# Kernel optimization log

Hardware: AMD Instinct MI355X
Metric: run time of the kernel (lower is better)

The kernel has to match this reference:

```python
import jax, jax.numpy as jnp
import numpy as np
import math

N_HEADS = 16
D_MODEL = 1024
DK = D_MODEL // N_HEADS
B, S = 2, 2048


def setup_inputs() -> dict:
    key = jax.random.key(0)
    ks = jax.random.split(key, 11)
    scale_in = 1.0 / math.sqrt(D_MODEL)
    scale_o = 1.0 / math.sqrt(N_HEADS * DK)
    return {
        "query": jax.random.normal(ks[0], (B, S, D_MODEL), jnp.float32),
        "key": jax.random.normal(ks[1], (B, S, D_MODEL), jnp.float32),
        "value": jax.random.normal(ks[2], (B, S, D_MODEL), jnp.float32),
        # stacked per-head projection weights [H, d_model, dk], biases [H, dk]
        "Wq": jax.random.normal(ks[3], (N_HEADS, D_MODEL, DK), jnp.float32) * scale_in,
        "bq": jax.random.normal(ks[4], (N_HEADS, DK), jnp.float32) * scale_in,
        "Wk": jax.random.normal(ks[5], (N_HEADS, D_MODEL, DK), jnp.float32) * scale_in,
        "bk": jax.random.normal(ks[6], (N_HEADS, DK), jnp.float32) * scale_in,
        "Wv": jax.random.normal(ks[7], (N_HEADS, D_MODEL, DK), jnp.float32) * scale_in,
        "bv": jax.random.normal(ks[8], (N_HEADS, DK), jnp.float32) * scale_in,
        "Wo": jax.random.normal(ks[9], (N_HEADS * DK, D_MODEL), jnp.float32) * scale_o,
        "bo": jax.random.normal(ks[10], (D_MODEL,), jnp.float32) * scale_o,
    }


def reference(query, key, value, Wq, bq, Wk, bk, Wv, bv, Wo, bo):
    # Per-head linear projections, vectorized over heads: [B,H,S,dk]
    q = jnp.einsum("bsd,hdk->bhsk", query, Wq) + bq[None, :, None, :]
    k = jnp.einsum("bsd,hdk->bhsk", key, Wk) + bk[None, :, None, :]
    v = jnp.einsum("bsd,hdk->bhsk", value, Wv) + bv[None, :, None, :]
    # Scaled dot-product scores [B,H,S,S]
    scores = jnp.einsum("bhsk,bhtk->bhst", q, k) / jnp.sqrt(jnp.asarray(DK, q.dtype))
    # FAITHFUL to source: nn.Softmax(dim=0) -> softmax over the BATCH axis
    attn = jax.nn.softmax(scores, axis=0)
    out = jnp.einsum("bhst,bhtk->bhsk", attn, v)  # [B,H,S,dk]
    # concat heads along feature dim (torch.cat dim=2)
    concat = out.transpose(0, 2, 1, 3).reshape(query.shape[0], query.shape[1], N_HEADS * DK)
    return concat @ Wo + bo
```

## Files before the change

### kernel.cpp

```cpp
#include <hip/hip_runtime.h>
#include <hip/hip_bf16.h>

#define B_ 2
#define S_ 2048
#define D_ 1024
#define H_ 16
#define DK_ 64
#define BS_ (B_ * S_)

typedef unsigned int u32;
typedef unsigned short u16;
typedef __attribute__((ext_vector_type(8))) short bf16x8;
typedef __attribute__((ext_vector_type(4))) float f32x4;

typedef const __attribute__((address_space(1))) void glb_cv;
typedef __attribute__((address_space(3))) void lds_v;

__device__ __forceinline__ void async_cp16(const void* g, void* l) {
    __builtin_amdgcn_global_load_lds((glb_cv*)g, (lds_v*)l, 16, 0, 0);
}

__device__ __forceinline__ float bf2f(u16 v) {
    union { u32 u; float f; } c; c.u = ((u32)v) << 16; return c.f;
}
__device__ __forceinline__ u16 f2bf(float f) {
    union { float f; u32 u; } c; c.f = f;
    u32 u = c.u;
    return (u16)((u + 0x7fffu + ((u >> 16) & 1u)) >> 16);
}
__device__ __forceinline__ u32 pack2(float a, float b) {
    return (u32)f2bf(a) | ((u32)f2bf(b) << 16);
}
__device__ __forceinline__ u32 packtr(float lo, float hi) {
    union { float f; u32 u; } a, b; a.f = lo; b.f = hi;
    return __builtin_amdgcn_perm(b.u, a.u, 0x07060302u);
}
__device__ __forceinline__ int sw64(int r, int c8) { return (((c8) + (r)) & 7) * 8; }

struct PrepArgs {
    const float* W[4]; u16* WT[4];
    const float* X[3]; u16* XB[3];
};
__global__ __launch_bounds__(256) void prep(PrepArgs a)
{
    const int id = blockIdx.x;
    const int tid = threadIdx.x;
    if (id >= 1024) {
        const int cid = id - 1024;
        const int z = cid >> 11;
        const size_t base = (size_t)(cid & 2047) * 2048 + tid * 8;
        const float* X = a.X[z];
        float4 x0 = *(const float4*)(X + base);
        float4 x1 = *(const float4*)(X + base + 4);
        uint4 o;
        o.x = pack2(x0.x, x0.y); o.y = pack2(x0.z, x0.w);
        o.z = pack2(x1.x, x1.y); o.w = pack2(x1.z, x1.w);
        *(uint4*)(a.XB[z] + base) = o;
        return;
    }
    __shared__ __attribute__((aligned(16))) u16 T[64][72];
    const int z = id >> 8;
    const int rem = id & 255;
    const float* W = a.W[z];
    u16* WT = a.WT[z];
    const int headMode = (z < 3) ? 1 : 0;
    const int k0 = (rem >> 4) * 64;
    const int n0 = (rem & 15) * 64;
    const int kr = tid >> 4;
    const int n4 = (tid & 15) * 4;
    #pragma unroll
    for (int pass = 0; pass < 4; ++pass) {
        int kk = k0 + pass * 16 + kr;
        const float* p = headMode
            ? (W + (size_t)((n0 + n4) >> 6) * (1024 * 64) + kk * 64 + ((n0 + n4) & 63))
            : (W + (size_t)kk * 1024 + n0 + n4);
        float4 v = *(const float4*)p;
        int krel = pass * 16 + kr;
        T[n4 + 0][krel] = f2bf(v.x);
        T[n4 + 1][krel] = f2bf(v.y);
        T[n4 + 2][krel] = f2bf(v.z);
        T[n4 + 3][krel] = f2bf(v.w);
    }
    __syncthreads();
    const int nr = tid >> 2;
    const int kq = (tid & 3) * 16;
    uint4 o0 = *(const uint4*)&T[nr][kq];
    uint4 o1 = *(const uint4*)&T[nr][kq + 8];
    u16* q = WT + (size_t)(n0 + nr) * 1024 + k0 + kq;
    *(uint4*)q = o0;
    *(uint4*)(q + 8) = o1;
}

__global__ __launch_bounds__(256) void vprep(
    const u16* __restrict__ Vb, u16* __restrict__ VT)
{
    __shared__ __attribute__((aligned(16))) u16 T[64][72];
    const int tid = threadIdx.x;
    const int t0 = blockIdx.x * 64;
    const int bh = blockIdx.y;
    const int b = bh >> 4, h = bh & 15;
    const int tr = tid >> 4;
    const int d4 = (tid & 15) * 4;
    #pragma unroll
    for (int pass = 0; pass < 4; ++pass) {
        int tt = t0 + pass * 16 + tr;
        const u16* p = Vb + (size_t)(b * S_ + tt) * 1024 + h * 64 + d4;
        u32 a = *(const u32*)p;
        u32 c = *(const u32*)(p + 2);
        int trel = pass * 16 + tr;
        T[d4 + 0][trel] = (u16)a;
        T[d4 + 1][trel] = (u16)(a >> 16);
        T[d4 + 2][trel] = (u16)c;
        T[d4 + 3][trel] = (u16)(c >> 16);
    }
    __syncthreads();
    const int dr = tid >> 2;
    const int tq = (tid & 3) * 16;
    uint4 o0 = *(const uint4*)&T[dr][tq];
    uint4 o1 = *(const uint4*)&T[dr][tq + 8];
    u16* q = VT + ((size_t)bh * 64 + dr) * 2048 + t0 + tq;
    *(uint4*)q = o0;
    *(uint4*)(q + 8) = o1;
}

struct ProjArgs {
    const u16* X[3];
    const u16* W[3];
    const float* bias[3];
    u16* Y[3];
};
__global__ __launch_bounds__(256) void proj3(ProjArgs pa)
{
    __shared__ __attribute__((aligned(16))) u16 As[128][32];
    __shared__ __attribute__((aligned(16))) u16 Bs[128][32];
    const int z = blockIdx.z;
    const u16* X = pa.X[z];
    const u16* WT = pa.W[z];
    const float* bias = pa.bias[z];
    u16* Y = pa.Y[z];
    const int neg = (z == 1);

    const int tid = threadIdx.x;
    const int lane = tid & 63;
    const int wave = tid >> 6;
    const int quad = lane >> 4;
    const int l16 = lane & 15;
    const int m0 = blockIdx.x * 128;
    const int n0 = blockIdx.y * 128;
    const int wm = (wave & 1) * 64, wn = (wave >> 1) * 64;

    f32x4 acc[4][4] = {};

    for (int k0 = 0; k0 < 1024; k0 += 32) {
        __syncthreads();
        #pragma unroll
        for (int call = 0; call < 2; ++call) {
            const int c = tid + call * 256;
            const int row = c >> 2, cc = (c & 3) * 8;
            char* la = (char*)&As[0][0] + (size_t)(c & ~63) * 16;
            async_cp16(X + (size_t)(m0 + row) * 1024 + k0 + cc, la);
            char* lb = (char*)&Bs[0][0] + (size_t)(c & ~63) * 16;
            async_cp16(WT + (size_t)(n0 + row) * 1024 + k0 + cc, lb);
        }
        __syncthreads();

        bf16x8 af[4], bfr[4];
        #pragma unroll
        for (int mt = 0; mt < 4; ++mt)
            af[mt] = *(const bf16x8*)&As[wm + mt * 16 + l16][quad * 8];
        #pragma unroll
        for (int nt = 0; nt < 4; ++nt)
            bfr[nt] = *(const bf16x8*)&Bs[wn + nt * 16 + l16][quad * 8];
        #pragma unroll
        for (int mt = 0; mt < 4; ++mt)
            #pragma unroll
            for (int nt = 0; nt < 4; ++nt)
                acc[mt][nt] = __builtin_amdgcn_mfma_f32_16x16x32_bf16(
                    af[mt], bfr[nt], acc[mt][nt], 0, 0, 0);
    }

    #pragma unroll
    for (int nt = 0; nt < 4; ++nt) {
        const int col = n0 + wn + nt * 16 + l16;
        const float bv = bias[col];
        #pragma unroll
        for (int mt = 0; mt < 4; ++mt) {
            #pragma unroll
            for (int r = 0; r < 4; ++r) {
                const int row = m0 + wm + mt * 16 + quad * 4 + r;
                float v = acc[mt][nt][r] + bv;
                if (neg && row >= 2048) v = -v;
                Y[(size_t)row * 1024 + col] = f2bf(v);
            }
        }
    }
}

__global__ __launch_bounds__(256) void gemm_out(
    const u16* __restrict__ P0, const u16* __restrict__ P1,
    const float* __restrict__ csP,
    const u16* __restrict__ WT, const float* __restrict__ bias,
    float* __restrict__ Y)
{
    __shared__ __attribute__((aligned(16))) u16 Aa[128][32];
    __shared__ __attribute__((aligned(16))) u16 Ab[128][32];
    __shared__ __attribute__((aligned(16))) u16 As[128][32];
    __shared__ __attribute__((aligned(16))) u16 Bs[64][32];
    __shared__ __attribute__((aligned(16))) float csL[1024];

    const int tid = threadIdx.x;
    const int lane = tid & 63;
    const int wave = tid >> 6;
    const int quad = lane >> 4;
    const int l16 = lane & 15;
    const int m0 = blockIdx.x * 128;
    const int n0 = blockIdx.y * 64;
    const int wm = (wave & 1) * 64, wn = (wave >> 1) * 32;
    const bool hiB = (m0 >= 2048);

    {
        const int t4 = tid * 4;
        float4 c0 = *(const float4*)(csP + t4);
        float4 c1 = *(const float4*)(csP + 1024 + t4);
        csL[t4 + 0] = c0.x + c1.x;
        csL[t4 + 1] = c0.y + c1.y;
        csL[t4 + 2] = c0.z + c1.z;
        csL[t4 + 3] = c0.w + c1.w;
    }

    f32x4 acc[4][2] = {};

    for (int k0 = 0; k0 < 1024; k0 += 32) {
        __syncthreads();
        #pragma unroll
        for (int call = 0; call < 2; ++call) {
            const int c = tid + call * 256;
            const int row = c >> 2, cc = (c & 3) * 8;
            char* la = (char*)&Aa[0][0] + (size_t)(c & ~63) * 16;
            async_cp16(P0 + (size_t)(m0 + row) * 1024 + k0 + cc, la);
            char* lb = (char*)&Ab[0][0] + (size_t)(c & ~63) * 16;
            async_cp16(P1 + (size_t)(m0 + row) * 1024 + k0 + cc, lb);
        }
        {
            const int c = tid;
            const int row = c >> 2, cc = (c & 3) * 8;
            char* lb = (char*)&Bs[0][0] + (size_t)(c & ~63) * 16;
            async_cp16(WT + (size_t)(n0 + row) * 1024 + k0 + cc, lb);
        }
        __syncthreads();

        #pragma unroll
        for (int call = 0; call < 2; ++call) {
            const int c = tid + call * 256;
            const int row = c >> 2, cc = (c & 3) * 8;
            bf16x8 av = *(const bf16x8*)&Aa[row][cc];
            bf16x8 bv2 = *(const bf16x8*)&Ab[row][cc];
            float v[8];
            #pragma unroll
            for (int jj = 0; jj < 8; ++jj)
                v[jj] = bf2f((u16)av[jj]) + bf2f((u16)bv2[jj]);
            if (hiB) {
                float4 c0 = *(const float4*)&csL[k0 + cc];
                float4 c1 = *(const float4*)&csL[k0 + cc + 4];
                v[0] = c0.x - v[0]; v[1] = c0.y - v[1];
                v[2] = c0.z - v[2]; v[3] = c0.w - v[3];
                v[4] = c1.x - v[4]; v[5] = c1.y - v[5];
                v[6] = c1.z - v[6]; v[7] = c1.w - v[7];
            }
            uint4 o;
            o.x = pack2(v[0], v[1]); o.y = pack2(v[2], v[3]);
            o.z = pack2(v[4], v[5]); o.w = pack2(v[6], v[7]);
            *(uint4*)&As[row][cc] = o;
        }
        __syncthreads();

        bf16x8 af[4], bfr[2];
        #pragma unroll
        for (int mt = 0; mt < 4; ++mt)
            af[mt] = *(const bf16x8*)&As[wm + mt * 16 + l16][quad * 8];
        #pragma unroll
        for (int nt = 0; nt < 2; ++nt)
            bfr[nt] = *(const bf16x8*)&Bs[wn + nt * 16 + l16][quad * 8];
        #pragma unroll
        for (int mt = 0; mt < 4; ++mt)
            #pragma unroll
            for (int nt = 0; nt < 2; ++nt)
                acc[mt][nt] = __builtin_amdgcn_mfma_f32_16x16x32_bf16(
                    af[mt], bfr[nt], acc[mt][nt], 0, 0, 0);
    }

    #pragma unroll
    for (int nt = 0; nt < 2; ++nt) {
        const int col = n0 + wn + nt * 16 + l16;
        const float bv = bias[col];
        #pragma unroll
        for (int mt = 0; mt < 4; ++mt) {
            #pragma unroll
            for (int r = 0; r < 4; ++r) {
                const int row = m0 + wm + mt * 16 + quad * 4 + r;
                Y[(size_t)row * 1024 + col] = acc[mt][nt][r] + bv;
            }
        }
    }
}

__global__ __launch_bounds__(256) void attn_mfma(
    const u16* __restrict__ Qb, const u16* __restrict__ Kb,
    const u16* __restrict__ VT, float* __restrict__ csP,
    u16* __restrict__ P0, u16* __restrict__ P1)
{
    __shared__ __attribute__((aligned(16))) u16 Ks[2][2][64][64];
    __shared__ __attribute__((aligned(16))) u16 Vs[2][2][64][64];
    __shared__ __attribute__((aligned(16))) u16 Ps[128][64];

    const int id = blockIdx.x;
    const int xcd = id & 7;
    const int rj = id >> 3;
    const int h = xcd * 2 + (rj >> 5);
    const int half = (rj >> 4) & 1;
    const int st = rj & 15;
    const int s0 = st * 128;
    const int tbase = half * 1024;
    u16* Pout = half ? P1 : P0;

    const int tid = threadIdx.x;
    const int lane = tid & 63;
    const int wave = tid >> 6;
    const int quad = lane >> 4;
    const int l16 = lane & 15;
    const int sr8 = lane >> 3;
    const int sc8 = lane & 7;

    auto stage = [&](int buf, int t0) {
        #pragma unroll
        for (int c = 0; c < 4; ++c) {
            const int kc = c * 4 + wave;
            const int bb = kc >> 3, row0 = (kc & 7) * 8;
            const int rr = row0 + sr8;
            const int cg = (sc8 - rr) & 7;
            async_cp16(Kb + (size_t)(bb * S_ + tbase + t0 + rr) * 1024 + h * 64 + cg * 8,
                       &Ks[buf][bb][row0][0]);
            async_cp16(VT + ((size_t)(bb * H_ + h) * 64 + rr) * 2048 + tbase + t0 + cg * 8,
                       &Vs[buf][bb][row0][0]);
        }
    };

    bf16x8 qf[2][2][2];
    #pragma unroll
    for (int sg = 0; sg < 2; ++sg)
        #pragma unroll
        for (int b = 0; b < 2; ++b)
            #pragma unroll
            for (int ks = 0; ks < 2; ++ks)
                qf[sg][b][ks] = *(const bf16x8*)(Qb
                    + (size_t)(b * S_ + s0 + wave * 32 + sg * 16 + l16) * 1024
                    + h * 64 + ks * 32 + quad * 8);

    f32x4 O0[2][4] = {}, T1[2][4] = {};
    float cacc = 0.f;

    stage(0, 0);
    __syncthreads();
    int cur = 0;
    for (int t0 = 0; t0 < 1024; t0 += 64) {
        if (t0 + 64 < 1024) stage(cur ^ 1, t0 + 64);

        f32x4 dacc[2][4] = {};
        __builtin_amdgcn_s_setprio(1);
        #pragma unroll
        for (int mt = 0; mt < 4; ++mt) {
            const int kr = mt * 16 + l16;
            #pragma unroll
            for (int ks = 0; ks < 2; ++ks) {
                bf16x8 k0f = *(const bf16x8*)&Ks[cur][0][kr][sw64(kr, ks * 4 + quad)];
                bf16x8 k1f = *(const bf16x8*)&Ks[cur][1][kr][sw64(kr, ks * 4 + quad)];
                #pragma unroll
                for (int sg = 0; sg < 2; ++sg) {
                    dacc[sg][mt] = __builtin_amdgcn_mfma_f32_16x16x32_bf16(
                        k0f, qf[sg][0][ks], dacc[sg][mt], 0, 0, 0);
                    dacc[sg][mt] = __builtin_amdgcn_mfma_f32_16x16x32_bf16(
                        k1f, qf[sg][1][ks], dacc[sg][mt], 0, 0, 0);
                }
            }
        }
        __builtin_amdgcn_s_setprio(0);

        #pragma unroll
        for (int sg = 0; sg < 2; ++sg) {
            const int pr = wave * 32 + sg * 16 + l16;
            #pragma unroll
            for (int mt = 0; mt < 4; ++mt) {
                float p[4];
                #pragma unroll
                for (int rr = 0; rr < 4; ++rr) {
                    float e = __expf(dacc[sg][mt][rr] * -0.125f);
                    p[rr] = __builtin_amdgcn_rcpf(1.0f + e);
                }
                uint2 w;
                w.x = packtr(p[0], p[1]);
                w.y = packtr(p[2], p[3]);
                const int c8 = 2 * mt + (quad >> 1);
                *(uint2*)&Ps[pr][sw64(pr, c8) + (quad & 1) * 4] = w;
            }
        }

        if (st == 0) {
            const int dk = tid >> 2, tp = tid & 3;
            bf16x8 vA = *(const bf16x8*)&Vs[cur][1][dk][sw64(dk, tp * 2)];
            bf16x8 vB = *(const bf16x8*)&Vs[cur][1][dk][sw64(dk, tp * 2 + 1)];
            #pragma unroll
            for (int jj = 0; jj < 8; ++jj)
                cacc += bf2f((u16)vA[jj]) + bf2f((u16)vB[jj]);
        }

        bf16x8 pf[2][2];
        #pragma unroll
        for (int sg = 0; sg < 2; ++sg) {
            const int pr = wave * 32 + sg * 16 + l16;
            pf[sg][0] = *(const bf16x8*)&Ps[pr][sw64(pr, quad)];
            pf[sg][1] = *(const bf16x8*)&Ps[pr][sw64(pr, 4 + quad)];
        }
        __builtin_amdgcn_s_setprio(1);
        #pragma unroll
        for (int nt = 0; nt < 4; ++nt) {
            const int vr = nt * 16 + l16;
            bf16x8 v00 = *(const bf16x8*)&Vs[cur][0][vr][sw64(vr, quad)];
            bf16x8 v01 = *(const bf16x8*)&Vs[cur][0][vr][sw64(vr, 4 + quad)];
            bf16x8 v10 = *(const bf16x8*)&Vs[cur][1][vr][sw64(vr, quad)];
            bf16x8 v11 = *(const bf16x8*)&Vs[cur][1][vr][sw64(vr, 4 + quad)];
            #pragma unroll
            for (int sg = 0; sg < 2; ++sg) {
                O0[sg][nt] = __builtin_amdgcn_mfma_f32_16x16x32_bf16(pf[sg][0], v00, O0[sg][nt], 0, 0, 0);
                O0[sg][nt] = __builtin_amdgcn_mfma_f32_16x16x32_bf16(pf[sg][1], v01, O0[sg][nt], 0, 0, 0);
                T1[sg][nt] = __builtin_amdgcn_mfma_f32_16x16x32_bf16(pf[sg][0], v10, T1[sg][nt], 0, 0, 0);
                T1[sg][nt] = __builtin_amdgcn_mfma_f32_16x16x32_bf16(pf[sg][1], v11, T1[sg][nt], 0, 0, 0);
            }
        }
        __builtin_amdgcn_s_setprio(0);
        __syncthreads();
        cur ^= 1;
    }

    #pragma unroll
    for (int sg = 0; sg < 2; ++sg)
        #pragma unroll
        for (int nt = 0; nt < 4; ++nt) {
            const int dk = nt * 16 + l16;
            #pragma unroll
            for (int rr = 0; rr < 4; ++rr) {
                const int s = s0 + wave * 32 + sg * 16 + quad * 4 + rr;
                Pout[(size_t)(0 * S_ + s) * 1024 + h * 64 + dk] = f2bf(O0[sg][nt][rr]);
                Pout[(size_t)(1 * S_ + s) * 1024 + h * 64 + dk] = f2bf(T1[sg][nt][rr]);
            }
        }

    if (st == 0) {
        cacc += __shfl_xor(cacc, 1);
        cacc += __shfl_xor(cacc, 2);
        if ((tid & 3) == 0)
            csP[half * 1024 + h * 64 + (tid >> 2)] = cacc;
    }
}

extern "C" void kernel_launch(void* const* d_in, const int* in_sizes, int n_in,
                              void* d_out, int out_size, void* d_ws, size_t ws_size,
                              hipStream_t stream) {
    const float* q  = (const float*)d_in[0];
    const float* k  = (const float*)d_in[1];
    const float* v  = (const float*)d_in[2];
    const float* Wq = (const float*)d_in[3];
    const float* bq = (const float*)d_in[4];
    const float* Wk = (const float*)d_in[5];
    const float* bk = (const float*)d_in[6];
    const float* Wv = (const float*)d_in[7];
    const float* bv = (const float*)d_in[8];
    const float* Wo = (const float*)d_in[9];
    const float* bo = (const float*)d_in[10];

    char* ws = (char*)d_ws;
    const size_t MB = 1024 * 1024;
    u16* Xq  = (u16*)(ws);
    float* csP = (float*)(ws);
    u16* WqT = (u16*)(ws + 8  * MB);
    u16* WkT = (u16*)(ws + 10 * MB);
    u16* WvT = (u16*)(ws + 12 * MB);
    u16* WoT = (u16*)(ws + 14 * MB);
    u16* Qp  = (u16*)(ws + 16 * MB);
    u16* Kp  = (u16*)(ws + 24 * MB);
    u16* Vp  = (u16*)(ws + 32 * MB);
    u16* Pa  = (u16*)(ws + 32 * MB);
    u16* VTv = (u16*)(ws + 40 * MB);
    u16* Xk  = (u16*)(ws + 40 * MB);
    u16* Xv  = (u16*)(ws + 48 * MB);
    u16* Pb  = (u16*)(ws + 48 * MB);

    dim3 blk(256);

    PrepArgs pr;
    pr.W[0] = Wq; pr.W[1] = Wk; pr.W[2] = Wv; pr.W[3] = Wo;
    pr.WT[0] = WqT; pr.WT[1] = WkT; pr.WT[2] = WvT; pr.WT[3] = WoT;
    pr.X[0] = q; pr.X[1] = k; pr.X[2] = v;
    pr.XB[0] = Xq; pr.XB[1] = Xk; pr.XB[2] = Xv;
    prep<<<dim3(1024 + 6144), blk, 0, stream>>>(pr);

    ProjArgs pa;
    pa.X[0] = Xq; pa.X[1] = Xk; pa.X[2] = Xv;
    pa.W[0] = WqT; pa.W[1] = WkT; pa.W[2] = WvT;
    pa.bias[0] = bq; pa.bias[1] = bk; pa.bias[2] = bv;
    pa.Y[0] = Qp; pa.Y[1] = Kp; pa.Y[2] = Vp;
    proj3<<<dim3(32, 8, 3), blk, 0, stream>>>(pa);

    vprep<<<dim3(32, 32), blk, 0, stream>>>(Vp, VTv);
    attn_mfma<<<dim3(512), blk, 0, stream>>>(Qp, Kp, VTv, csP, Pa, Pb);
    gemm_out<<<dim3(32, 16), blk, 0, stream>>>(Pa, Pb, csP, WoT, bo, (float*)d_out);
}
```

Measured before the change: 238.5 us.

## Fuse V transpose into projection epilogue and drop LDS staging in output GEMM

The V projection now writes its output directly in the transposed [b,h,d,t] layout from the GEMM epilogue, which removes the separate vprep kernel launch and its round trip through global memory. proj3 now loads 64-wide K slices per barrier pair using two LDS buffers, which halves the number of synchronisations. gemm_out builds its combined A fragments in registers instead of writing them to LDS and re-reading them, which removes one barrier per k-step. The transposed V stores are strided 8-byte writes, and the workspace buffers are reassigned so that they do not alias in the new flow.

```diff
diff --git a/kernel.cpp b/kernel.cpp
--- a/kernel.cpp
+++ b/kernel.cpp
@@ -91,38 +91,6 @@
     *(uint4*)(q + 8) = o1;
 }
 
-__global__ __launch_bounds__(256) void vprep(
-    const u16* __restrict__ Vb, u16* __restrict__ VT)
-{
-    __shared__ __attribute__((aligned(16))) u16 T[64][72];
-    const int tid = threadIdx.x;
-    const int t0 = blockIdx.x * 64;
-    const int bh = blockIdx.y;
-    const int b = bh >> 4, h = bh & 15;
-    const int tr = tid >> 4;
-    const int d4 = (tid & 15) * 4;
-    #pragma unroll
-    for (int pass = 0; pass < 4; ++pass) {
-        int tt = t0 + pass * 16 + tr;
-        const u16* p = Vb + (size_t)(b * S_ + tt) * 1024 + h * 64 + d4;
-        u32 a = *(const u32*)p;
-        u32 c = *(const u32*)(p + 2);
-        int trel = pass * 16 + tr;
-        T[d4 + 0][trel] = (u16)a;
-        T[d4 + 1][trel] = (u16)(a >> 16);
-        T[d4 + 2][trel] = (u16)c;
-        T[d4 + 3][trel] = (u16)(c >> 16);
-    }
-    __syncthreads();
-    const int dr = tid >> 2;
-    const int tq = (tid & 3) * 16;
-    uint4 o0 = *(const uint4*)&T[dr][tq];
-    uint4 o1 = *(const uint4*)&T[dr][tq + 8];
-    u16* q = VT + ((size_t)bh * 64 + dr) * 2048 + t0 + tq;
-    *(uint4*)q = o0;
-    *(uint4*)(q + 8) = o1;
-}
-
 struct ProjArgs {
     const u16* X[3];
     const u16* W[3];
@@ -131,8 +99,8 @@
 };
 __global__ __launch_bounds__(256) void proj3(ProjArgs pa)
 {
-    __shared__ __attribute__((aligned(16))) u16 As[128][32];
-    __shared__ __attribute__((aligned(16))) u16 Bs[128][32];
+    __shared__ __attribute__((aligned(16))) u16 As[2][128][32];
+    __shared__ __attribute__((aligned(16))) u16 Bs[2][128][32];
     const int z = blockIdx.z;
     const u16* X = pa.X[z];
     const u16* WT = pa.W[z];
@@ -151,32 +119,57 @@
 
     f32x4 acc[4][4] = {};
 
-    for (int k0 = 0; k0 < 1024; k0 += 32) {
+    for (int k0 = 0; k0 < 1024; k0 += 64) {
         __syncthreads();
         #pragma unroll
-        for (int call = 0; call < 2; ++call) {
-            const int c = tid + call * 256;
-            const int row = c >> 2, cc = (c & 3) * 8;
-            char* la = (char*)&As[0][0] + (size_t)(c & ~63) * 16;
-            async_cp16(X + (size_t)(m0 + row) * 1024 + k0 + cc, la);
-            char* lb = (char*)&Bs[0][0] + (size_t)(c & ~63) * 16;
-            async_cp16(WT + (size_t)(n0 + row) * 1024 + k0 + cc, lb);
-        }
+        for (int ks = 0; ks < 2; ++ks)
+            #pragma unroll
+            for (int call = 0; call < 2; ++call) {
+                const int c = tid + call * 256;
+                const int row = c >> 2, cc = (c & 3) * 8;
+                char* la = (char*)&As[ks][0][0] + (size_t)(c & ~63) * 16;
+                async_cp16(X + (size_t)(m0 + row) * 1024 + k0 + ks * 32 + cc, la);
+                char* lb = (char*)&Bs[ks][0][0] + (size_t)(c & ~63) * 16;
+                async_cp16(WT + (size_t)(n0 + row) * 1024 + k0 + ks * 32 + cc, lb);
+            }
         __syncthreads();
 
-        bf16x8 af[4], bfr[4];
-        #pragma unroll
-        for (int mt = 0; mt < 4; ++mt)
-            af[mt] = *(const bf16x8*)&As[wm + mt * 16 + l16][quad * 8];
-        #pragma unroll
-        for (int nt = 0; nt < 4; ++nt)
-            bfr[nt] = *(const bf16x8*)&Bs[wn + nt * 16 + l16][quad * 8];
-        #pragma unroll
-        for (int mt = 0; mt < 4; ++mt)
+        #pragma unroll
+        for (int ks = 0; ks < 2; ++ks) {
+            bf16x8 af[4], bfr[4];
+            #pragma unroll
+            for (int mt = 0; mt < 4; ++mt)
+                af[mt] = *(const bf16x8*)&As[ks][wm + mt * 16 + l16][quad * 8];
             #pragma unroll
             for (int nt = 0; nt < 4; ++nt)
-                acc[mt][nt] = __builtin_amdgcn_mfma_f32_16x16x32_bf16(
-                    af[mt], bfr[nt], acc[mt][nt], 0, 0, 0);
+                bfr[nt] = *(const bf16x8*)&Bs[ks][wn + nt * 16 + l16][quad * 8];
+            #pragma unroll
+            for (int mt = 0; mt < 4; ++mt)
+                #pragma unroll
+                for (int nt = 0; nt < 4; ++nt)
+                    acc[mt][nt] = __builtin_amdgcn_mfma_f32_16x16x32_bf16(
+                        af[mt], bfr[nt], acc[mt][nt], 0, 0, 0);
+        }
+    }
+
+    if (z == 2) {
+        #pragma unroll
+        for (int nt = 0; nt < 4; ++nt) {
+            const int col = n0 + wn + nt * 16 + l16;
+            const float bv = bias[col];
+            u16* vrow = Y + ((size_t)(col >> 6) * 64 + (col & 63)) * 2048;
+            #pragma unroll
+            for (int mt = 0; mt < 4; ++mt) {
+                const int row = m0 + wm + mt * 16 + quad * 4;
+                const size_t boff = (size_t)(row >> 11) * (16 * 64 * 2048);
+                const int t = row & 2047;
+                uint2 w;
+                w.x = pack2(acc[mt][nt][0] + bv, acc[mt][nt][1] + bv);
+                w.y = pack2(acc[mt][nt][2] + bv, acc[mt][nt][3] + bv);
+                *(uint2*)(vrow + boff + t) = w;
+            }
+        }
+        return;
     }
 
     #pragma unroll
@@ -204,7 +197,6 @@
 {
     __shared__ __attribute__((aligned(16))) u16 Aa[128][32];
     __shared__ __attribute__((aligned(16))) u16 Ab[128][32];
-    __shared__ __attribute__((aligned(16))) u16 As[128][32];
     __shared__ __attribute__((aligned(16))) u16 Bs[64][32];
     __shared__ __attribute__((aligned(16))) float csL[1024];
 
@@ -249,35 +241,30 @@
         }
         __syncthreads();
 
-        #pragma unroll
-        for (int call = 0; call < 2; ++call) {
-            const int c = tid + call * 256;
-            const int row = c >> 2, cc = (c & 3) * 8;
-            bf16x8 av = *(const bf16x8*)&Aa[row][cc];
-            bf16x8 bv2 = *(const bf16x8*)&Ab[row][cc];
+        float4 cs0, cs1;
+        if (hiB) {
+            cs0 = *(const float4*)&csL[k0 + quad * 8];
+            cs1 = *(const float4*)&csL[k0 + quad * 8 + 4];
+        }
+        bf16x8 af[4], bfr[2];
+        #pragma unroll
+        for (int mt = 0; mt < 4; ++mt) {
+            bf16x8 aa = *(const bf16x8*)&Aa[wm + mt * 16 + l16][quad * 8];
+            bf16x8 ab = *(const bf16x8*)&Ab[wm + mt * 16 + l16][quad * 8];
             float v[8];
             #pragma unroll
             for (int jj = 0; jj < 8; ++jj)
-                v[jj] = bf2f((u16)av[jj]) + bf2f((u16)bv2[jj]);
+                v[jj] = bf2f((u16)aa[jj]) + bf2f((u16)ab[jj]);
             if (hiB) {
-                float4 c0 = *(const float4*)&csL[k0 + cc];
-                float4 c1 = *(const float4*)&csL[k0 + cc + 4];
-                v[0] = c0.x - v[0]; v[1] = c0.y - v[1];
-                v[2] = c0.z - v[2]; v[3] = c0.w - v[3];
-                v[4] = c1.x - v[4]; v[5] = c1.y - v[5];
-                v[6] = c1.z - v[6]; v[7] = c1.w - v[7];
-            }
-            uint4 o;
-            o.x = pack2(v[0], v[1]); o.y = pack2(v[2], v[3]);
-            o.z = pack2(v[4], v[5]); o.w = pack2(v[6], v[7]);
-            *(uint4*)&As[row][cc] = o;
-        }
-        __syncthreads();
-
-        bf16x8 af[4], bfr[2];
-        #pragma unroll
-        for (int mt = 0; mt < 4; ++mt)
-            af[mt] = *(const bf16x8*)&As[wm + mt * 16 + l16][quad * 8];
+                v[0] = cs0.x - v[0]; v[1] = cs0.y - v[1];
+                v[2] = cs0.z - v[2]; v[3] = cs0.w - v[3];
+                v[4] = cs1.x - v[4]; v[5] = cs1.y - v[5];
+                v[6] = cs1.z - v[6]; v[7] = cs1.w - v[7];
+            }
+            u32* rp = (u32*)&af[mt];
+            rp[0] = pack2(v[0], v[1]); rp[1] = pack2(v[2], v[3]);
+            rp[2] = pack2(v[4], v[5]); rp[3] = pack2(v[6], v[7]);
+        }
         #pragma unroll
         for (int nt = 0; nt < 2; ++nt)
             bfr[nt] = *(const bf16x8*)&Bs[wn + nt * 16 + l16][quad * 8];
@@ -487,12 +474,11 @@
     u16* WoT = (u16*)(ws + 14 * MB);
     u16* Qp  = (u16*)(ws + 16 * MB);
     u16* Kp  = (u16*)(ws + 24 * MB);
-    u16* Vp  = (u16*)(ws + 32 * MB);
-    u16* Pa  = (u16*)(ws + 32 * MB);
-    u16* VTv = (u16*)(ws + 40 * MB);
+    u16* VTv = (u16*)(ws + 32 * MB);
     u16* Xk  = (u16*)(ws + 40 * MB);
+    u16* Pb  = (u16*)(ws + 40 * MB);
     u16* Xv  = (u16*)(ws + 48 * MB);
-    u16* Pb  = (u16*)(ws + 48 * MB);
+    u16* Pa  = (u16*)(ws + 48 * MB);
 
     dim3 blk(256);
 
@@ -507,10 +493,9 @@
     pa.X[0] = Xq; pa.X[1] = Xk; pa.X[2] = Xv;
     pa.W[0] = WqT; pa.W[1] = WkT; pa.W[2] = WvT;
     pa.bias[0] = bq; pa.bias[1] = bk; pa.bias[2] = bv;
-    pa.Y[0] = Qp; pa.Y[1] = Kp; pa.Y[2] = Vp;
+    pa.Y[0] = Qp; pa.Y[1] = Kp; pa.Y[2] = VTv;
     proj3<<<dim3(32, 8, 3), blk, 0, stream>>>(pa);
 
-    vprep<<<dim3(32, 32), blk, 0, stream>>>(Vp, VTv);
     attn_mfma<<<dim3(512), blk, 0, stream>>>(Qp, Kp, VTv, csP, Pa, Pb);
     gemm_out<<<dim3(32, 16), blk, 0, stream>>>(Pa, Pb, csP, WoT, bo, (float*)d_out);
 }
```

After: 249.1 us. 1.04x slower.
